# Optimization experiments

Measured on AMD Instinct MI355X. Metric: run time of the kernel, lower is better.

Reference implementation:

```python
import jax, jax.numpy as jnp
import numpy as np

SCALE = 8      # scale_factor from map_to_mat_info
PATCH = 32     # up_delta - low_delta + 1 == right_delta - left_delta + 1 (uniform interior patches)


def setup_inputs() -> dict:
    key = jax.random.key(0)
    mat_h, mat_w = 160, 160
    H = (mat_h - 1) * SCALE + PATCH  # 1304: deltas (0,31,0,31) -> no border clipping
    W = (mat_w - 1) * SCALE + PATCH
    x = jax.random.normal(key, (1, 3, H, W), dtype=jnp.float32)
    rgb_weight = jnp.array([0.299, 0.587, 0.114], dtype=jnp.float32).reshape(1, 3, 1, 1)
    return {"x": x, "rgb_weight": rgb_weight, "mat_h": mat_h, "mat_w": mat_w}


def reference(x, rgb_weight, mat_h, mat_w):
    P = PATCH
    # RGB -> grayscale (convert_gray branch for in_channels == 3)
    gray = jnp.sum(x * rgb_weight, axis=1)[0]  # (H, W)
    # Gather all overlapping PxP patches at stride SCALE -> (mat_h, mat_w, P, P)
    rows = (jnp.arange(mat_h) * SCALE)[:, None] + jnp.arange(P)[None, :]  # (mat_h, P)
    cols = (jnp.arange(mat_w) * SCALE)[:, None] + jnp.arange(P)[None, :]  # (mat_w, P)
    p = gray[rows.reshape(-1)].reshape(mat_h, P, -1)              # (mat_h, P, W)
    p = p[:, :, cols.reshape(-1)].reshape(mat_h, P, mat_w, P)     # (mat_h, P, mat_w, P)
    patches = jnp.transpose(p, (0, 2, 1, 3))                      # (mat_h, mat_w, P, P)
    # torch.rfft(signal_ndim=2, onesided=False) == full 2D FFT; power = re^2 + im^2
    F = jnp.fft.fft2(patches)
    log_power = jnp.log(F.real * F.real + F.imag * F.imag + 1.0)
    # High-frequency region sums (h == w == P, static)
    lo = P // 2 - P // 4 - 1   # 7
    up = P // 2 + P // 4       # 24
    r1 = jnp.sum(log_power[..., lo:up + 1, :], axis=(-2, -1))
    r2 = jnp.sum(log_power[..., up + 1:, lo:up + 1], axis=(-2, -1))
    r3 = jnp.sum(log_power[..., :lo, lo:up + 1], axis=(-2, -1))
    mat = (r1 + r2 + r3)[None, None]  # (1, 1, mat_h, mat_w)
    return mat / jnp.max(mat)
```

## Files before the change

### kernel.cpp

```cpp
#include <hip/hip_runtime.h>
#include <math.h>

#define SCALE 8
#define PSZ 32

__device__ constexpr float C32[16] = {
     1.000000000000000f,  0.980785280403230f,  0.923879532511287f,  0.831469612302545f,
     0.707106781186548f,  0.555570233019602f,  0.382683432365090f,  0.195090322016128f,
     0.000000000000000f, -0.195090322016128f, -0.382683432365090f, -0.555570233019602f,
    -0.707106781186548f, -0.831469612302545f, -0.923879532511287f, -0.980785280403230f };
__device__ constexpr float S32[16] = {
     0.000000000000000f,  0.195090322016128f,  0.382683432365090f,  0.555570233019602f,
     0.707106781186548f,  0.831469612302545f,  0.923879532511287f,  0.980785280403230f,
     1.000000000000000f,  0.980785280403230f,  0.923879532511287f,  0.831469612302545f,
     0.707106781186548f,  0.555570233019602f,  0.382683432365090f,  0.195090322016128f };

__device__ __forceinline__ constexpr int brev5(int i) {
    return ((i & 1) << 4) | ((i & 2) << 2) | (i & 4) | ((i & 8) >> 2) | ((i & 16) >> 4);
}

__device__ __forceinline__ void fft32(float re[PSZ], float im[PSZ]) {
#pragma unroll
    for (int i = 0; i < 32; ++i) {
        const int j = brev5(i);
        if (j > i) {
            float t = re[i]; re[i] = re[j]; re[j] = t;
            t = im[i]; im[i] = im[j]; im[j] = t;
        }
    }
#pragma unroll
    for (int s = 1; s <= 5; ++s) {
        const int m = 1 << s;
        const int h = m >> 1;
        const int tstep = 32 >> s;
#pragma unroll
        for (int k = 0; k < 32; k += m) {
#pragma unroll
            for (int j = 0; j < h; ++j) {
                const float wr = C32[j * tstep];
                const float wi = -S32[j * tstep];
                const int a = k + j;
                const int b = k + j + h;
                const float tr = wr * re[b] - wi * im[b];
                const float ti = wr * im[b] + wi * re[b];
                re[b] = re[a] - tr; im[b] = im[a] - ti;
                re[a] = re[a] + tr; im[a] = im[a] + ti;
            }
        }
    }
}

__device__ __forceinline__ unsigned pack_bf2(float hi, float lo) {
    const unsigned uh = __float_as_uint(hi) + 0x8000u;
    const unsigned ul = __float_as_uint(lo) + 0x8000u;
    return (uh & 0xFFFF0000u) | (ul >> 16);
}
__device__ __forceinline__ float bf_hi(unsigned u) { return __uint_as_float(u & 0xFFFF0000u); }
__device__ __forceinline__ float bf_lo(unsigned u) { return __uint_as_float(u << 16); }

__global__ __launch_bounds__(256) void gray_kernel(
        const float* __restrict__ x, const float* __restrict__ w,
        float* __restrict__ g, int n4, long long HW) {
    const int i = blockIdx.x * 256 + threadIdx.x;
    if (i >= n4) return;
    const float w0 = w[0], w1 = w[1], w2 = w[2];
    const float4 a = reinterpret_cast<const float4*>(x)[i];
    const float4 b = reinterpret_cast<const float4*>(x + HW)[i];
    const float4 c = reinterpret_cast<const float4*>(x + 2 * HW)[i];
    float4 o;
    o.x = w0 * a.x + w1 * b.x + w2 * c.x;
    o.y = w0 * a.y + w1 * b.y + w2 * c.y;
    o.z = w0 * a.z + w1 * b.z + w2 * c.z;
    o.w = w0 * a.w + w1 * b.w + w2 * c.w;
    reinterpret_cast<float4*>(g)[i] = o;
}

template <bool GRAY_PRE>
__global__ __launch_bounds__(128, 4) void hfdft_patch_kernel(
        const float* __restrict__ x, const float* __restrict__ w,
        float* __restrict__ out, int H, int W, int mat_h, int mat_w) {
    __shared__ unsigned cb[8 * 528];

    const int tid = threadIdx.x;
    const int wid = tid >> 6;
    const int lane = tid & 63;
    const int P0 = blockIdx.x * 8 + wid * 4;
    const int total = mat_h * mat_w;
    const long long HW = (long long)H * W;
    unsigned* cbw = cb + wid * 4 * 528;

    {
        const int g = lane >> 5, r = lane & 31;
        int pA = P0 + 2 * g;
        if (pA > total - 1) pA = total - 1;
        int pB = pA + 1; if (pB > total - 1) pB = total - 1;
        const int phA = pA / mat_w, pwA = pA % mat_w;
        const int phB = pB / mat_w, pwB = pB % mat_w;
        const bool adj = (phA == phB) && (pwB == pwA + 1);

        float re[PSZ], im[PSZ];
        if (GRAY_PRE) {
            if (adj) {
                const int base = (phA * SCALE + r) * W + pwA * SCALE;
                const float4* g4 = reinterpret_cast<const float4*>(x + base);
                float win[40];
#pragma unroll
                for (int q = 0; q < 10; ++q) {
                    const float4 v = g4[q];
                    win[4 * q + 0] = v.x; win[4 * q + 1] = v.y;
                    win[4 * q + 2] = v.z; win[4 * q + 3] = v.w;
                }
#pragma unroll
                for (int i = 0; i < PSZ; ++i) { re[i] = win[i]; im[i] = win[i + 8]; }
            } else {
                const int baseA = (phA * SCALE + r) * W + pwA * SCALE;
                const int baseB = (phB * SCALE + r) * W + pwB * SCALE;
#pragma unroll
                for (int i = 0; i < PSZ; ++i) { re[i] = x[baseA + i]; im[i] = x[baseB + i]; }
            }
        } else {
            const float w0 = w[0], w1 = w[1], w2 = w[2];
            if (adj && ((W & 3) == 0)) {
                const int base = (phA * SCALE + r) * W + pwA * SCALE;
                const float4* a4 = reinterpret_cast<const float4*>(x + base);
                const float4* b4 = reinterpret_cast<const float4*>(x + HW + base);
                const float4* c4 = reinterpret_cast<const float4*>(x + 2 * HW + base);
                float win[40];
#pragma unroll
                for (int q = 0; q < 10; ++q) {
                    const float4 a = a4[q], b = b4[q], c = c4[q];
                    win[4 * q + 0] = w0 * a.x + w1 * b.x + w2 * c.x;
                    win[4 * q + 1] = w0 * a.y + w1 * b.y + w2 * c.y;
                    win[4 * q + 2] = w0 * a.z + w1 * b.z + w2 * c.z;
                    win[4 * q + 3] = w0 * a.w + w1 * b.w + w2 * c.w;
                }
#pragma unroll
                for (int i = 0; i < PSZ; ++i) { re[i] = win[i]; im[i] = win[i + 8]; }
            } else {
                const int baseA = (phA * SCALE + r) * W + pwA * SCALE;
                const int baseB = (phB * SCALE + r) * W + pwB * SCALE;
#pragma unroll
                for (int i = 0; i < PSZ; ++i) {
                    re[i] = w0 * x[baseA + i] + w1 * x[HW + baseA + i] + w2 * x[2 * HW + baseA + i];
                    im[i] = w0 * x[baseB + i] + w1 * x[HW + baseB + i] + w2 * x[2 * HW + baseB + i];
                }
            }
        }

        fft32(re, im);

        unsigned* cbA = cbw + (2 * g) * 528;
        unsigned* cbB = cbA + 528;
        cbA[r] = pack_bf2(re[0], re[16]);
        cbB[r] = pack_bf2(im[0], im[16]);
#pragma unroll
        for (int k = 1; k <= 15; ++k) {
            const int m = 32 - k;
            const float far_ = 0.5f * (re[k] + re[m]);
            const float fai_ = 0.5f * (im[k] - im[m]);
            const float fbr_ = 0.5f * (im[k] + im[m]);
            const float fbi_ = 0.5f * (re[m] - re[k]);
            cbA[k * 33 + r] = pack_bf2(far_, fai_);
            cbB[k * 33 + r] = pack_bf2(fbr_, fbi_);
        }
    }

    asm volatile("s_waitcnt lgkmcnt(0)" ::: "memory");

    {
        const int pl = lane >> 4, slot = lane & 15;
        const int p = P0 + pl;
        const unsigned* cbp = cbw + pl * 528 + slot * 33;

        float cre[PSZ], cim[PSZ];
#pragma unroll
        for (int r2 = 0; r2 < PSZ; ++r2) {
            const unsigned u = cbp[r2];
            cre[r2] = bf_hi(u);
            cim[r2] = bf_lo(u);
        }

        fft32(cre, cim);

        float s0 = 0.0f, s1 = 0.0f;
        if (slot == 0) {
#pragma unroll
            for (int kr = 0; kr <= 16; ++kr) {
                const int m = (32 - kr) & 31;
                const float g0r = 0.5f * (cre[kr] + cre[m]);
                const float g0i = 0.5f * (cim[kr] - cim[m]);
                const float g1r = 0.5f * (cim[kr] + cim[m]);
                const float g1i = 0.5f * (cre[m] - cre[kr]);
                const float w0c = (kr >= 7 ? 1.0f : 0.0f) + ((kr >= 8 && kr <= 15) ? 1.0f : 0.0f);
                const float w16c = 1.0f + ((kr >= 1 && kr <= 15) ? 1.0f : 0.0f);
                if (w0c > 0.0f)
                    s0 = fmaf(w0c, __logf(g0r * g0r + g0i * g0i + 1.0f), s0);
                s1 = fmaf(w16c, __logf(g1r * g1r + g1i * g1i + 1.0f), s1);
            }
        } else {
            const float b1f = (slot >= 7) ? 1.0f : 0.0f;
            const float m1f = (slot >= 8) ? 1.0f : 0.0f;
#pragma unroll
            for (int kr = 0; kr < 32; ++kr) {
                const float lp = __logf(cre[kr] * cre[kr] + cim[kr] * cim[kr] + 1.0f);
                float wgt;
                if (kr >= 8 && kr <= 24)      wgt = 2.0f;
                else if (kr == 7)             wgt = 1.0f + m1f;
                else if (kr == 25)            wgt = b1f + 1.0f;
                else                          wgt = b1f + m1f;
                if (kr & 1) s1 = fmaf(wgt, lp, s1);
                else        s0 = fmaf(wgt, lp, s0);
            }
        }
        float s = s0 + s1;

#pragma unroll
        for (int off = 8; off >= 1; off >>= 1) s += __shfl_xor(s, off, 16);
        if (slot == 0 && p < total) out[p] = s;
    }
}

__global__ __launch_bounds__(1024) void max_kernel(
        const float* __restrict__ sums, int n, float* __restrict__ partial) {
    __shared__ float sm[16];
    float m = 0.0f;
    for (int i = blockIdx.x * 1024 + threadIdx.x; i < n; i += gridDim.x * 1024)
        m = fmaxf(m, sums[i]);
#pragma unroll
    for (int off = 32; off >= 1; off >>= 1) m = fmaxf(m, __shfl_xor(m, off, 64));
    if ((threadIdx.x & 63) == 0) sm[threadIdx.x >> 6] = m;
    __syncthreads();
    if (threadIdx.x == 0) {
#pragma unroll
        for (int i = 1; i < 16; ++i) m = fmaxf(m, sm[i]);
        partial[blockIdx.x] = m;
    }
}

__global__ __launch_bounds__(256) void norm_kernel(
        float* __restrict__ out, int n, const float* __restrict__ partial) {
    const int i = blockIdx.x * 256 + threadIdx.x;
    float m = partial[0];
#pragma unroll
    for (int b = 1; b < 8; ++b) m = fmaxf(m, partial[b]);
    if (i < n) out[i] = out[i] / m;
}

extern "C" void kernel_launch(void* const* d_in, const int* in_sizes, int n_in,
                              void* d_out, int out_size, void* d_ws, size_t ws_size,
                              hipStream_t stream) {
    const float* x = (const float*)d_in[0];
    const float* w = (const float*)d_in[1];
    float* out = (float*)d_out;

    const int HWi = in_sizes[0] / 3;
    const int H = (int)(sqrt((double)HWi) + 0.5);
    const int W = H;
    const long long HW = (long long)H * W;
    const int mat = (int)(sqrt((double)out_size) + 0.5);
    const int total = mat * mat;
    const int blocksA = (total + 7) / 8;

    float* partial = (float*)d_ws;
    float* gray = (float*)((char*)d_ws + 256);
    const size_t need = 256 + (size_t)HW * 4;

    if (ws_size >= need && (W & 3) == 0) {
        const int n4 = (int)(HW / 4);
        hipLaunchKernelGGL(gray_kernel, dim3((n4 + 255) / 256), dim3(256), 0, stream,
                           x, w, gray, n4, HW);
        hipLaunchKernelGGL((hfdft_patch_kernel<true>), dim3(blocksA), dim3(128), 0, stream,
                           gray, w, out, H, W, mat, mat);
    } else {
        hipLaunchKernelGGL((hfdft_patch_kernel<false>), dim3(blocksA), dim3(128), 0, stream,
                           x, w, out, H, W, mat, mat);
    }
    hipLaunchKernelGGL(max_kernel, dim3(8), dim3(1024), 0, stream, out, total, partial);
    hipLaunchKernelGGL(norm_kernel, dim3((total + 255) / 256), dim3(256), 0, stream,
                       out, total, partial);
}
```

Baseline: 44.85 us.

## Split 32-point FFTs into two radix-2 decimated 16-point FFT halves

Replaces each 32-point register FFT, in both the row and column passes, with a decimation-in-frequency split. The even and odd output bins are each computed by a 16-point FFT on sums and on twiddled differences, processed one half after the other. This roughly halves the live register arrays, which should cut register pressure and spilling. The __launch_bounds__ min-blocks hint is dropped. The cost is reloading the input window from global memory and the column data from LDS twice, plus more complex weighting logic.

Measured after the change: 46.02 us. +2.6%, slower.

```diff
diff --git a/kernel.cpp b/kernel.cpp
--- a/kernel.cpp
+++ b/kernel.cpp
@@ -15,26 +15,26 @@
      1.000000000000000f,  0.980785280403230f,  0.923879532511287f,  0.831469612302545f,
      0.707106781186548f,  0.555570233019602f,  0.382683432365090f,  0.195090322016128f };
 
-__device__ __forceinline__ constexpr int brev5(int i) {
-    return ((i & 1) << 4) | ((i & 2) << 2) | (i & 4) | ((i & 8) >> 2) | ((i & 16) >> 4);
-}
-
-__device__ __forceinline__ void fft32(float re[PSZ], float im[PSZ]) {
-#pragma unroll
-    for (int i = 0; i < 32; ++i) {
-        const int j = brev5(i);
+__device__ __forceinline__ constexpr int brev4(int i) {
+    return ((i & 1) << 3) | ((i & 2) << 1) | ((i & 4) >> 1) | ((i & 8) >> 3);
+}
+
+__device__ __forceinline__ void fft16(float re[16], float im[16]) {
+#pragma unroll
+    for (int i = 0; i < 16; ++i) {
+        const int j = brev4(i);
         if (j > i) {
             float t = re[i]; re[i] = re[j]; re[j] = t;
             t = im[i]; im[i] = im[j]; im[j] = t;
         }
     }
 #pragma unroll
-    for (int s = 1; s <= 5; ++s) {
+    for (int s = 1; s <= 4; ++s) {
         const int m = 1 << s;
         const int h = m >> 1;
         const int tstep = 32 >> s;
 #pragma unroll
-        for (int k = 0; k < 32; k += m) {
+        for (int k = 0; k < 16; k += m) {
 #pragma unroll
             for (int j = 0; j < h; ++j) {
                 const float wr = C32[j * tstep];
@@ -76,7 +76,7 @@
 }
 
 template <bool GRAY_PRE>
-__global__ __launch_bounds__(128, 4) void hfdft_patch_kernel(
+__global__ __launch_bounds__(128) void hfdft_patch_kernel(
         const float* __restrict__ x, const float* __restrict__ w,
         float* __restrict__ out, int H, int W, int mat_h, int mat_w) {
     __shared__ unsigned cb[8 * 528];
@@ -97,71 +97,129 @@
         const int phA = pA / mat_w, pwA = pA % mat_w;
         const int phB = pB / mat_w, pwB = pB % mat_w;
         const bool adj = (phA == phB) && (pwB == pwA + 1);
-
-        float re[PSZ], im[PSZ];
-        if (GRAY_PRE) {
-            if (adj) {
-                const int base = (phA * SCALE + r) * W + pwA * SCALE;
-                const float4* g4 = reinterpret_cast<const float4*>(x + base);
-                float win[40];
+        const int baseA = (phA * SCALE + r) * W + pwA * SCALE;
+        const int baseB = (phB * SCALE + r) * W + pwB * SCALE;
+        const float w0 = GRAY_PRE ? 0.0f : w[0];
+        const float w1 = GRAY_PRE ? 0.0f : w[1];
+        const float w2 = GRAY_PRE ? 0.0f : w[2];
+
+        unsigned* cbA = cbw + (2 * g) * 528;
+        unsigned* cbB = cbA + 528;
+
+
+        {
+            float win[40];
+            if (GRAY_PRE && adj) {
+                const float4* g4 = reinterpret_cast<const float4*>(x + baseA);
 #pragma unroll
                 for (int q = 0; q < 10; ++q) {
                     const float4 v = g4[q];
                     win[4 * q + 0] = v.x; win[4 * q + 1] = v.y;
                     win[4 * q + 2] = v.z; win[4 * q + 3] = v.w;
                 }
-#pragma unroll
-                for (int i = 0; i < PSZ; ++i) { re[i] = win[i]; im[i] = win[i + 8]; }
-            } else {
-                const int baseA = (phA * SCALE + r) * W + pwA * SCALE;
-                const int baseB = (phB * SCALE + r) * W + pwB * SCALE;
-#pragma unroll
-                for (int i = 0; i < PSZ; ++i) { re[i] = x[baseA + i]; im[i] = x[baseB + i]; }
-            }
-        } else {
-            const float w0 = w[0], w1 = w[1], w2 = w[2];
-            if (adj && ((W & 3) == 0)) {
-                const int base = (phA * SCALE + r) * W + pwA * SCALE;
-                const float4* a4 = reinterpret_cast<const float4*>(x + base);
-                const float4* b4 = reinterpret_cast<const float4*>(x + HW + base);
-                const float4* c4 = reinterpret_cast<const float4*>(x + 2 * HW + base);
-                float win[40];
+            } else if (GRAY_PRE) {
+#pragma unroll
+                for (int i = 0; i < 32; ++i) win[i] = x[baseA + i];
+#pragma unroll
+                for (int i = 0; i < 8; ++i) win[32 + i] = 0.0f;
+            } else {
+#pragma unroll
+                for (int i = 0; i < 32; ++i)
+                    win[i] = w0 * x[baseA + i] + w1 * x[HW + baseA + i] + w2 * x[2 * HW + baseA + i];
+#pragma unroll
+                for (int i = 0; i < 8; ++i) win[32 + i] = 0.0f;
+            }
+            float er[16], ei[16];
+            if (GRAY_PRE && adj) {
+#pragma unroll
+                for (int i = 0; i < 16; ++i) {
+                    er[i] = win[i] + win[i + 16];
+                    ei[i] = win[i + 8] + win[i + 24];
+                }
+            } else if (GRAY_PRE) {
+#pragma unroll
+                for (int i = 0; i < 16; ++i) {
+                    er[i] = win[i] + win[i + 16];
+                    ei[i] = x[baseB + i] + x[baseB + i + 16];
+                }
+            } else {
+#pragma unroll
+                for (int i = 0; i < 16; ++i) {
+                    er[i] = win[i] + win[i + 16];
+                    const float blo = w0 * x[baseB + i] + w1 * x[HW + baseB + i] + w2 * x[2 * HW + baseB + i];
+                    const float bhi = w0 * x[baseB + i + 16] + w1 * x[HW + baseB + i + 16] + w2 * x[2 * HW + baseB + i + 16];
+                    ei[i] = blo + bhi;
+                }
+            }
+            fft16(er, ei);
+            cbA[r] = pack_bf2(er[0], er[8]);
+            cbB[r] = pack_bf2(ei[0], ei[8]);
+#pragma unroll
+            for (int k2 = 1; k2 <= 7; ++k2) {
+                const int e1 = k2, e2 = 16 - k2;
+                const float far_ = 0.5f * (er[e1] + er[e2]);
+                const float fai_ = 0.5f * (ei[e1] - ei[e2]);
+                const float fbr_ = 0.5f * (ei[e1] + ei[e2]);
+                const float fbi_ = 0.5f * (er[e2] - er[e1]);
+                cbA[(2 * k2) * 33 + r] = pack_bf2(far_, fai_);
+                cbB[(2 * k2) * 33 + r] = pack_bf2(fbr_, fbi_);
+            }
+        }
+
+        asm volatile("" ::: "memory");
+
+        {
+            float win[40];
+            if (GRAY_PRE && adj) {
+                const float4* g4 = reinterpret_cast<const float4*>(x + baseA);
 #pragma unroll
                 for (int q = 0; q < 10; ++q) {
-                    const float4 a = a4[q], b = b4[q], c = c4[q];
-                    win[4 * q + 0] = w0 * a.x + w1 * b.x + w2 * c.x;
-                    win[4 * q + 1] = w0 * a.y + w1 * b.y + w2 * c.y;
-                    win[4 * q + 2] = w0 * a.z + w1 * b.z + w2 * c.z;
-                    win[4 * q + 3] = w0 * a.w + w1 * b.w + w2 * c.w;
-                }
-#pragma unroll
-                for (int i = 0; i < PSZ; ++i) { re[i] = win[i]; im[i] = win[i + 8]; }
-            } else {
-                const int baseA = (phA * SCALE + r) * W + pwA * SCALE;
-                const int baseB = (phB * SCALE + r) * W + pwB * SCALE;
-#pragma unroll
-                for (int i = 0; i < PSZ; ++i) {
-                    re[i] = w0 * x[baseA + i] + w1 * x[HW + baseA + i] + w2 * x[2 * HW + baseA + i];
-                    im[i] = w0 * x[baseB + i] + w1 * x[HW + baseB + i] + w2 * x[2 * HW + baseB + i];
-                }
-            }
-        }
-
-        fft32(re, im);
-
-        unsigned* cbA = cbw + (2 * g) * 528;
-        unsigned* cbB = cbA + 528;
-        cbA[r] = pack_bf2(re[0], re[16]);
-        cbB[r] = pack_bf2(im[0], im[16]);
-#pragma unroll
-        for (int k = 1; k <= 15; ++k) {
-            const int m = 32 - k;
-            const float far_ = 0.5f * (re[k] + re[m]);
-            const float fai_ = 0.5f * (im[k] - im[m]);
-            const float fbr_ = 0.5f * (im[k] + im[m]);
-            const float fbi_ = 0.5f * (re[m] - re[k]);
-            cbA[k * 33 + r] = pack_bf2(far_, fai_);
-            cbB[k * 33 + r] = pack_bf2(fbr_, fbi_);
+                    const float4 v = g4[q];
+                    win[4 * q + 0] = v.x; win[4 * q + 1] = v.y;
+                    win[4 * q + 2] = v.z; win[4 * q + 3] = v.w;
+                }
+            } else if (GRAY_PRE) {
+#pragma unroll
+                for (int i = 0; i < 32; ++i) win[i] = x[baseA + i];
+#pragma unroll
+                for (int i = 0; i < 8; ++i) win[32 + i] = 0.0f;
+            } else {
+#pragma unroll
+                for (int i = 0; i < 32; ++i)
+                    win[i] = w0 * x[baseA + i] + w1 * x[HW + baseA + i] + w2 * x[2 * HW + baseA + i];
+#pragma unroll
+                for (int i = 0; i < 8; ++i) win[32 + i] = 0.0f;
+            }
+            float orr[16], oi[16];
+#pragma unroll
+            for (int i = 0; i < 16; ++i) {
+                float dre, dim;
+                if (GRAY_PRE && adj) {
+                    dre = win[i] - win[i + 16];
+                    dim = win[i + 8] - win[i + 24];
+                } else if (GRAY_PRE) {
+                    dre = win[i] - win[i + 16];
+                    dim = x[baseB + i] - x[baseB + i + 16];
+                } else {
+                    dre = win[i] - win[i + 16];
+                    const float blo = w0 * x[baseB + i] + w1 * x[HW + baseB + i] + w2 * x[2 * HW + baseB + i];
+                    const float bhi = w0 * x[baseB + i + 16] + w1 * x[HW + baseB + i + 16] + w2 * x[2 * HW + baseB + i + 16];
+                    dim = blo - bhi;
+                }
+                orr[i] = dre * C32[i] + dim * S32[i];
+                oi[i]  = dim * C32[i] - dre * S32[i];
+            }
+            fft16(orr, oi);
+#pragma unroll
+            for (int k2 = 0; k2 <= 7; ++k2) {
+                const int o1 = k2, o2 = 15 - k2;
+                const float far_ = 0.5f * (orr[o1] + orr[o2]);
+                const float fai_ = 0.5f * (oi[o1] - oi[o2]);
+                const float fbr_ = 0.5f * (oi[o1] + oi[o2]);
+                const float fbi_ = 0.5f * (orr[o2] - orr[o1]);
+                cbA[(2 * k2 + 1) * 33 + r] = pack_bf2(far_, fai_);
+                cbB[(2 * k2 + 1) * 33 + r] = pack_bf2(fbr_, fbi_);
+            }
         }
     }
 
@@ -171,49 +229,92 @@
         const int pl = lane >> 4, slot = lane & 15;
         const int p = P0 + pl;
         const unsigned* cbp = cbw + pl * 528 + slot * 33;
-
-        float cre[PSZ], cim[PSZ];
-#pragma unroll
-        for (int r2 = 0; r2 < PSZ; ++r2) {
-            const unsigned u = cbp[r2];
-            cre[r2] = bf_hi(u);
-            cim[r2] = bf_lo(u);
-        }
-
-        fft32(cre, cim);
+        const float b1f = (slot >= 7) ? 1.0f : 0.0f;
+        const float m1f = (slot >= 8) ? 1.0f : 0.0f;
 
         float s0 = 0.0f, s1 = 0.0f;
-        if (slot == 0) {
-#pragma unroll
-            for (int kr = 0; kr <= 16; ++kr) {
-                const int m = (32 - kr) & 31;
-                const float g0r = 0.5f * (cre[kr] + cre[m]);
-                const float g0i = 0.5f * (cim[kr] - cim[m]);
-                const float g1r = 0.5f * (cim[kr] + cim[m]);
-                const float g1i = 0.5f * (cre[m] - cre[kr]);
-                const float w0c = (kr >= 7 ? 1.0f : 0.0f) + ((kr >= 8 && kr <= 15) ? 1.0f : 0.0f);
-                const float w16c = 1.0f + ((kr >= 1 && kr <= 15) ? 1.0f : 0.0f);
-                if (w0c > 0.0f)
-                    s0 = fmaf(w0c, __logf(g0r * g0r + g0i * g0i + 1.0f), s0);
-                s1 = fmaf(w16c, __logf(g1r * g1r + g1i * g1i + 1.0f), s1);
-            }
-        } else {
-            const float b1f = (slot >= 7) ? 1.0f : 0.0f;
-            const float m1f = (slot >= 8) ? 1.0f : 0.0f;
-#pragma unroll
-            for (int kr = 0; kr < 32; ++kr) {
-                const float lp = __logf(cre[kr] * cre[kr] + cim[kr] * cim[kr] + 1.0f);
-                float wgt;
-                if (kr >= 8 && kr <= 24)      wgt = 2.0f;
-                else if (kr == 7)             wgt = 1.0f + m1f;
-                else if (kr == 25)            wgt = b1f + 1.0f;
-                else                          wgt = b1f + m1f;
-                if (kr & 1) s1 = fmaf(wgt, lp, s1);
-                else        s0 = fmaf(wgt, lp, s0);
-            }
-        }
+
+        {
+            float er[16], ei[16];
+#pragma unroll
+            for (int i = 0; i < 16; ++i) {
+                const unsigned u0 = cbp[i], u1 = cbp[i + 16];
+                er[i] = bf_hi(u0) + bf_hi(u1);
+                ei[i] = bf_lo(u0) + bf_lo(u1);
+            }
+            fft16(er, ei);
+            if (slot == 0) {
+#pragma unroll
+                for (int k2 = 0; k2 <= 8; ++k2) {
+                    const int kr = 2 * k2;
+                    const int a = k2, b = (k2 == 0) ? 0 : 16 - k2;
+                    const float g0r = 0.5f * (er[a] + er[b]);
+                    const float g0i = 0.5f * (ei[a] - ei[b]);
+                    const float g1r = 0.5f * (ei[a] + ei[b]);
+                    const float g1i = 0.5f * (er[b] - er[a]);
+                    const float w0c = (kr >= 7 ? 1.0f : 0.0f) + ((kr >= 8 && kr <= 15) ? 1.0f : 0.0f);
+                    const float w16c = 1.0f + ((kr >= 1 && kr <= 15) ? 1.0f : 0.0f);
+                    if (w0c > 0.0f)
+                        s0 = fmaf(w0c, __logf(g0r * g0r + g0i * g0i + 1.0f), s0);
+                    s1 = fmaf(w16c, __logf(g1r * g1r + g1i * g1i + 1.0f), s1);
+                }
+            } else {
+#pragma unroll
+                for (int k2 = 0; k2 < 16; ++k2) {
+                    const int kr = 2 * k2;
+                    const float lp = __logf(er[k2] * er[k2] + ei[k2] * ei[k2] + 1.0f);
+                    const float wgt = (kr >= 8 && kr <= 24) ? 2.0f : (b1f + m1f);
+                    if (k2 & 1) s1 = fmaf(wgt, lp, s1);
+                    else        s0 = fmaf(wgt, lp, s0);
+                }
+            }
+        }
+
+        asm volatile("" ::: "memory");
+
+        {
+            float orr[16], oi[16];
+#pragma unroll
+            for (int i = 0; i < 16; ++i) {
+                const unsigned u0 = cbp[i], u1 = cbp[i + 16];
+                const float dre = bf_hi(u0) - bf_hi(u1);
+                const float dim = bf_lo(u0) - bf_lo(u1);
+                orr[i] = dre * C32[i] + dim * S32[i];
+                oi[i]  = dim * C32[i] - dre * S32[i];
+            }
+            fft16(orr, oi);
+            if (slot == 0) {
+#pragma unroll
+                for (int k2 = 0; k2 <= 7; ++k2) {
+                    const int kr = 2 * k2 + 1;
+                    const int a = k2, b = 15 - k2;
+                    const float g0r = 0.5f * (orr[a] + orr[b]);
+                    const float g0i = 0.5f * (oi[a] - oi[b]);
+                    const float g1r = 0.5f * (oi[a] + oi[b]);
+                    const float g1i = 0.5f * (orr[b] - orr[a]);
+                    const float w0c = (kr >= 7 ? 1.0f : 0.0f) + ((kr >= 8 && kr <= 15) ? 1.0f : 0.0f);
+                    const float w16c = 2.0f;
+                    if (w0c > 0.0f)
+                        s0 = fmaf(w0c, __logf(g0r * g0r + g0i * g0i + 1.0f), s0);
+                    s1 = fmaf(w16c, __logf(g1r * g1r + g1i * g1i + 1.0f), s1);
+                }
+            } else {
+#pragma unroll
+                for (int k2 = 0; k2 < 16; ++k2) {
+                    const int kr = 2 * k2 + 1;
+                    const float lp = __logf(orr[k2] * orr[k2] + oi[k2] * oi[k2] + 1.0f);
+                    float wgt;
+                    if (kr == 7)                   wgt = 1.0f + m1f;
+                    else if (kr == 25)             wgt = b1f + 1.0f;
+                    else if (kr >= 9 && kr <= 23)  wgt = 2.0f;
+                    else                           wgt = b1f + m1f;
+                    if (k2 & 1) s1 = fmaf(wgt, lp, s1);
+                    else        s0 = fmaf(wgt, lp, s0);
+                }
+            }
+        }
+
         float s = s0 + s1;
-
 #pragma unroll
         for (int off = 8; off >= 1; off >>= 1) s += __shfl_xor(s, off, 16);
         if (slot == 0 && p < total) out[p] = s;
```
